# Performance work log

Hardware: AMD Instinct MI355X
Metric: run time of the kernel (lower is better)

The kernel has to match this reference:

```python
import jax, jax.numpy as jnp
import numpy as np

ITERS = 3  # iteration_num in the original module
B, L, H, N_LABELS = 16, 64, 512, 64


def setup_inputs() -> dict:
    key = jax.random.key(0)
    ks = jax.random.split(key, 11)
    s = H ** -0.5
    s2 = (2 * H) ** -0.5
    return {
        "h": jax.random.normal(ks[0], (B, L, H), jnp.float32),
        "c_slot": jax.random.normal(ks[1], (B, L, H), jnp.float32),
        "c_inte": jax.random.normal(ks[2], (B, H), jnp.float32),
        "W_SF": jax.random.normal(ks[3], (H, H), jnp.float32) * s,
        "V_SF": jax.random.normal(ks[4], (H, H), jnp.float32) * s,
        "V1_ID": jax.random.normal(ks[5], (H, H), jnp.float32) * s,
        "V2_ID_w": jax.random.normal(ks[6], (H, H), jnp.float32) * s,
        "V2_ID_b": jax.random.normal(ks[7], (H,), jnp.float32) * s,
        "W_ID": jax.random.normal(ks[8], (H, H), jnp.float32) * s,
        "W_inte_ans": jax.random.normal(ks[9], (N_LABELS, 2 * H), jnp.float32) * s2,
        "W_slot_ans": jax.random.normal(ks[10], (N_LABELS, 2 * H), jnp.float32) * s2,
    }


def reference(h, c_slot, c_inte, W_SF, V_SF, V1_ID, V2_ID_w, V2_ID_b, W_ID,
              W_inte_ans, W_slot_ans):
    # h, c_slot: [B,L,H]; c_inte: [B,H]
    # slot_features (V2_ID(h)) is loop-invariant in the original; hoisted.
    slot_features = h @ V2_ID_w.T + V2_ID_b  # [B,L,H]
    r_inte = c_inte
    r_slot = None
    for _ in range(ITERS):
        # f = sum_i V_SF(tanh(c_slot[:,i] + W_SF(r_inte))); V_SF linear -> sum first
        t = jnp.tanh(c_slot + (r_inte @ W_SF.T)[:, None, :])  # [B,L,H]
        f = t.sum(axis=1) @ V_SF.T  # [B,H]
        r_slot = f[:, None, :] * c_slot  # [B,L,H]
        hid = r_slot @ V1_ID.T  # [B,L,H]
        # pairwise additive attention scores, summed over batch AND hidden dims
        u = jnp.tanh(hid[:, :, None, :] + slot_features[:, None, :, :])  # [B,L,L,H]
        s = jnp.exp(jnp.einsum('bijh,gh->bijg', u, W_ID)).sum(axis=(0, 3))  # [L,L]
        atts = jnp.diagonal(s) / s.sum(axis=1)  # [L], scalar per position
        r = jnp.einsum('i,bih->bh', atts, r_slot)  # [B,H]
        r_inte = r + c_inte
    intent_output = jnp.concatenate([r_inte, h[:, -1, :]], axis=1) @ W_inte_ans.T  # [B,n_labels]
    slot_output = jnp.concatenate([h, r_slot], axis=-1) @ W_slot_ans.T  # [B,L,n_labels]
    return intent_output, slot_output
```

## Files before the change

### kernel.cpp

```cpp
#include <hip/hip_runtime.h>
#include <math.h>


typedef __attribute__((ext_vector_type(8))) short bf16x8;
typedef __attribute__((ext_vector_type(4))) float f32x4;

__device__ inline short f2bf(float x) {
  unsigned u = __float_as_uint(x);
  unsigned r = (u + 0x7fffu + ((u >> 16) & 1u)) >> 16;
  return (short)r;
}
__device__ inline float bf2f(short s) {
  return __uint_as_float(((unsigned)(unsigned short)s) << 16);
}
__device__ inline unsigned pack2(float a, float b) {
  return (__float_as_uint(a) >> 16) | (__float_as_uint(b) & 0xffff0000u);
}
__device__ inline float ftanh(float x) {
  float t = __expf(2.f * x);
  return 1.f - 2.f * __builtin_amdgcn_rcpf(t + 1.f);
}
__device__ inline void split8(float4 a, float4 b, bf16x8* hi, bf16x8* lo) {
  float xs[8] = {a.x, a.y, a.z, a.w, b.x, b.y, b.z, b.w};
  bf16x8 h, l;
#pragma unroll
  for (int e = 0; e < 8; ++e) {
    short hh = f2bf(xs[e]);
    h[e] = hh;
    l[e] = f2bf(xs[e] - bf2f(hh));
  }
  *hi = h;
  *lo = l;
}

__global__ __launch_bounds__(256) void k_lin1(
    const float* __restrict__ A, const float* __restrict__ rawB,
    const float* __restrict__ bias, float* __restrict__ C,
    const float* __restrict__ W_ID, const float* __restrict__ V1,
    const float* __restrict__ W_ia, const float* __restrict__ W_sa,
    const float* __restrict__ W_SF, const float* __restrict__ V_SF,
    short* __restrict__ wbp, short* __restrict__ v1h, short* __restrict__ v1l,
    float* __restrict__ wia_t, float* __restrict__ wsa_t,
    float* __restrict__ wsf_t, float* __restrict__ vsf_t,
    float* __restrict__ fzero) {
  __shared__ short Ah[2][512], Al[2][512];
  __shared__ float tile[64][65];
  const int nh = blockIdx.y;
  const int t = threadIdx.x;

  if (nh >= 4) {
    const int pid = (nh - 4) * 64 + blockIdx.x;
    if (pid < 256) {
#pragma unroll
      for (int e = 0; e < 4; ++e) {
        int idx = pid * 1024 + e * 256 + t;
        int j = idx & 7, lane = (idx >> 3) & 63;
        int ntile = (idx >> 9) & 31, kstep = idx >> 14;
        int g = ntile * 16 + (lane & 15);
        int h = kstep * 32 + (lane >> 4) * 8 + j;
        wbp[idx] = f2bf(W_ID[g * 512 + h]);
      }
    } else if (pid < 512) {
      int p = pid - 256;
#pragma unroll
      for (int e = 0; e < 4; ++e) {
        int idx = p * 1024 + e * 256 + t;
        int j = idx & 7, lane = (idx >> 3) & 63;
        int ntile = (idx >> 9) & 31, kstep = idx >> 14;
        int g = ntile * 16 + (lane & 15);
        int h = kstep * 32 + (lane >> 4) * 8 + j;
        float x = V1[g * 512 + h];
        short hi = f2bf(x);
        v1h[idx] = hi;
        v1l[idx] = f2bf(x - bf2f(hi));
      }
    } else if (pid < 672) {
      int p = pid - 512;
      const float* tin;
      float* tout;
      int R, C2, c0, r0;
      if (p < 64) {
        tin = W_SF; tout = wsf_t; R = 512; C2 = 512;
        c0 = (p & 7) * 64; r0 = (p >> 3) * 64;
      } else if (p < 128) {
        int q = p - 64;
        tin = V_SF; tout = vsf_t; R = 512; C2 = 512;
        c0 = (q & 7) * 64; r0 = (q >> 3) * 64;
      } else if (p < 144) {
        tin = W_ia; tout = wia_t; R = 64; C2 = 1024;
        c0 = (p - 128) * 64; r0 = 0;
      } else {
        tin = W_sa; tout = wsa_t; R = 64; C2 = 1024;
        c0 = (p - 144) * 64; r0 = 0;
      }
      const int tx = t & 63, ty = t >> 6;
#pragma unroll
      for (int it2 = 0; it2 < 16; ++it2) {
        int rl = ty + it2 * 4;
        tile[rl][tx] = tin[(r0 + rl) * C2 + c0 + tx];
      }
      __syncthreads();
#pragma unroll
      for (int it2 = 0; it2 < 16; ++it2) {
        int cl = ty + it2 * 4;
        tout[(c0 + cl) * R + r0 + tx] = tile[tx][cl];
      }
    }
    return;
  }

  const int m0 = blockIdx.x * 16;
  if (fzero && nh == 1 && blockIdx.x < 16) {
    fzero[blockIdx.x * 512 + t] = 0.f;
    fzero[blockIdx.x * 512 + 256 + t] = 0.f;
  }
  const int w = t >> 6, lane = t & 63;
  const int lq = lane >> 4, lm = lane & 15;
  f32x4 acc[2];
#pragma unroll
  for (int c = 0; c < 2; ++c) acc[c] = (f32x4){0.f, 0.f, 0.f, 0.f};

  const int nt0 = nh * 8 + w * 2;
  const float* vb0 = rawB + (nt0 * 16 + lm) * 512 + lq * 8;
  const float* vb1 = vb0 + 16 * 512;

  const int la = t >> 2, j0 = (t & 3) * 2;
  const int m = la & 15, kk = (la >> 4) * 8 + j0;
  const float* abase = A + (m0 + m) * 512 + kk;
  float2 x = *(const float2*)abase;

  for (int ks = 0; ks < 16; ++ks) {
    const int buf = ks & 1;
    float4 q0 = *(const float4*)(vb0 + ks * 32);
    float4 q1 = *(const float4*)(vb0 + ks * 32 + 4);
    float4 p0 = *(const float4*)(vb1 + ks * 32);
    float4 p1 = *(const float4*)(vb1 + ks * 32 + 4);
    float2 xn = x;
    if (ks < 15) xn = *(const float2*)(abase + (ks + 1) * 32);
    short h0 = f2bf(x.x), h1 = f2bf(x.y);
    short l0 = f2bf(x.x - bf2f(h0)), l1 = f2bf(x.y - bf2f(h1));
    *(short2*)&Ah[buf][t * 2] = make_short2(h0, h1);
    *(short2*)&Al[buf][t * 2] = make_short2(l0, l1);
    bf16x8 b0h, b0l, b1h, b1l;
    split8(q0, q1, &b0h, &b0l);
    split8(p0, p1, &b1h, &b1l);
    __syncthreads();
    bf16x8 ah = *(const bf16x8*)&Ah[buf][lane * 8];
    bf16x8 al = *(const bf16x8*)&Al[buf][lane * 8];
    acc[0] = __builtin_amdgcn_mfma_f32_16x16x32_bf16(ah, b0h, acc[0], 0, 0, 0);
    acc[0] = __builtin_amdgcn_mfma_f32_16x16x32_bf16(al, b0h, acc[0], 0, 0, 0);
    acc[0] = __builtin_amdgcn_mfma_f32_16x16x32_bf16(ah, b0l, acc[0], 0, 0, 0);
    acc[1] = __builtin_amdgcn_mfma_f32_16x16x32_bf16(ah, b1h, acc[1], 0, 0, 0);
    acc[1] = __builtin_amdgcn_mfma_f32_16x16x32_bf16(al, b1h, acc[1], 0, 0, 0);
    acc[1] = __builtin_amdgcn_mfma_f32_16x16x32_bf16(ah, b1l, acc[1], 0, 0, 0);
    x = xn;
  }
#pragma unroll
  for (int c = 0; c < 2; ++c)
#pragma unroll
    for (int reg = 0; reg < 4; ++reg) {
      int mm = m0 + lq * 4 + reg;
      int n = (nt0 + c) * 16 + lm;
      C[mm * 512 + n] = acc[c][reg] + bias[n];
    }
}

__global__ __launch_bounds__(256) void k_lin(const float* __restrict__ c_slot,
                                             const float* __restrict__ f,
                                             const short* __restrict__ bh,
                                             const short* __restrict__ bl,
                                             float* __restrict__ C,
                                             float* __restrict__ rs_out,
                                             float* __restrict__ smat0) {
  __shared__ short Ah[2][512], Al[2][512];
  __shared__ float fl[512];
  const int m0 = blockIdx.x * 16;
  const int nh = blockIdx.y;
  const int t = threadIdx.x;
  if (nh == 0 && blockIdx.x < 8) {
    smat0[blockIdx.x * 512 + t] = 0.f;
    smat0[blockIdx.x * 512 + 256 + t] = 0.f;
  }
  fl[t] = f[(blockIdx.x >> 2) * 512 + t];
  fl[t + 256] = f[(blockIdx.x >> 2) * 512 + 256 + t];
  const int w = t >> 6, lane = t & 63;
  const int lq = lane >> 4, lm = lane & 15;
  f32x4 acc[2];
#pragma unroll
  for (int c = 0; c < 2; ++c) acc[c] = (f32x4){0.f, 0.f, 0.f, 0.f};

  const bf16x8* gbh = (const bf16x8*)bh + (nh * 8 + w * 2) * 64 + lane;
  const bf16x8* gbl = (const bf16x8*)bl + (nh * 8 + w * 2) * 64 + lane;

  const int la = t >> 2, j0 = (t & 3) * 2;
  const int m = la & 15, kk = (la >> 4) * 8 + j0;
  const float* abase = c_slot + (m0 + m) * 512 + kk;
  float* rbase = rs_out + (m0 + m) * 512 + kk;
  __syncthreads();
  float2 x = *(const float2*)abase;

  for (int ks = 0; ks < 16; ++ks) {
    const int buf = ks & 1;
    bf16x8 b0h = gbh[ks * 2048];
    bf16x8 b1h = gbh[ks * 2048 + 64];
    bf16x8 b0l = gbl[ks * 2048];
    bf16x8 b1l = gbl[ks * 2048 + 64];
    float2 xn = x;
    if (ks < 15) xn = *(const float2*)(abase + (ks + 1) * 32);
    float a0 = x.x * fl[ks * 32 + kk];
    float a1 = x.y * fl[ks * 32 + kk + 1];
    if (nh == 0) *(float2*)(rbase + ks * 32) = make_float2(a0, a1);
    short h0 = f2bf(a0), h1 = f2bf(a1);
    short l0 = f2bf(a0 - bf2f(h0)), l1 = f2bf(a1 - bf2f(h1));
    *(short2*)&Ah[buf][t * 2] = make_short2(h0, h1);
    *(short2*)&Al[buf][t * 2] = make_short2(l0, l1);
    __syncthreads();
    bf16x8 ah = *(const bf16x8*)&Ah[buf][lane * 8];
    bf16x8 al = *(const bf16x8*)&Al[buf][lane * 8];
    acc[0] = __builtin_amdgcn_mfma_f32_16x16x32_bf16(ah, b0h, acc[0], 0, 0, 0);
    acc[0] = __builtin_amdgcn_mfma_f32_16x16x32_bf16(al, b0h, acc[0], 0, 0, 0);
    acc[0] = __builtin_amdgcn_mfma_f32_16x16x32_bf16(ah, b0l, acc[0], 0, 0, 0);
    acc[1] = __builtin_amdgcn_mfma_f32_16x16x32_bf16(ah, b1h, acc[1], 0, 0, 0);
    acc[1] = __builtin_amdgcn_mfma_f32_16x16x32_bf16(al, b1h, acc[1], 0, 0, 0);
    acc[1] = __builtin_amdgcn_mfma_f32_16x16x32_bf16(ah, b1l, acc[1], 0, 0, 0);
    x = xn;
  }
#pragma unroll
  for (int c = 0; c < 2; ++c)
#pragma unroll
    for (int reg = 0; reg < 4; ++reg) {
      int mm = m0 + lq * 4 + reg;
      int n = nh * 128 + (w * 2 + c) * 16 + lm;
      C[mm * 512 + n] = acc[c][reg];
    }
}

__global__ __launch_bounds__(512) void k_mid(int first,
                                             const float* __restrict__ smat,
                                             const float* __restrict__ r_slot,
                                             const float* __restrict__ c_inte,
                                             const float* __restrict__ c_slot,
                                             const float* __restrict__ wsf_t,
                                             const float* __restrict__ vsf_t,
                                             float* __restrict__ f) {
  __shared__ float av[64];
  __shared__ float riv[512];
  __shared__ float red[512];
  __shared__ float tm[64], ts[64];
  const int b = blockIdx.x >> 3, hc = blockIdx.x & 7;
  const int t = threadIdx.x;
  const int hl = t & 63, kq = t >> 6;

  if (first) {
    riv[t] = c_inte[b * 512 + t];
  } else {
    if (t < 256) {
      int w = t >> 6, lane = t & 63;
      for (int r = w * 16; r < w * 16 + 16; ++r) {
        float v = smat[r * 64 + lane];
        float s = v;
        s += __shfl_xor(s, 1);
        s += __shfl_xor(s, 2);
        s += __shfl_xor(s, 4);
        s += __shfl_xor(s, 8);
        s += __shfl_xor(s, 16);
        s += __shfl_xor(s, 32);
        float d = __shfl(v, r);
        if (lane == 0) av[r] = d / s;
      }
    }
    __syncthreads();
    float a = 0.f;
    const float* rp = r_slot + b * 64 * 512 + t;
#pragma unroll 8
    for (int i = 0; i < 64; ++i) a += av[i] * rp[i * 512];
    riv[t] = a + c_inte[b * 512 + t];
  }
  __syncthreads();
  {
    const float* wp = wsf_t + hc * 64 + hl;
    float p = 0.f;
#pragma unroll 8
    for (int k = kq * 64; k < kq * 64 + 64; ++k) p += riv[k] * wp[k * 512];
    red[t] = p;
  }
  __syncthreads();
  if (t < 64) {
    float s = 0.f;
#pragma unroll
    for (int q = 0; q < 8; ++q) s += red[q * 64 + t];
    tm[t] = s;
  }
  __syncthreads();
  {
    float tmph = tm[hl];
    const float* cp = c_slot + (b * 64 + kq * 8) * 512 + hc * 64 + hl;
    float s = 0.f;
#pragma unroll
    for (int l = 0; l < 8; ++l) s += ftanh(cp[l * 512] + tmph);
    red[t] = s;
  }
  __syncthreads();
  if (t < 64) {
    float s = 0.f;
#pragma unroll
    for (int q = 0; q < 8; ++q) s += red[q * 64 + t];
    ts[t] = s;
  }
  __syncthreads();
  {
    const float* vp = vsf_t + (hc * 64) * 512 + t;
    float p = 0.f;
#pragma unroll 8
    for (int k = 0; k < 64; ++k) p += ts[k] * vp[k * 512];
    atomicAdd(&f[b * 512 + t], p);
  }
}

__global__ __launch_bounds__(512, 4) void k_score(const float* __restrict__ hid,
                                                  const float* __restrict__ sf,
                                                  const short* __restrict__ wbp,
                                                  float* __restrict__ smat,
                                                  float* __restrict__ fz,
                                                  float* __restrict__ oz) {
  __shared__ short As[16][2048];
  __shared__ float red[8][64];
  const int i = blockIdx.x, b = blockIdx.y;
  const int t = threadIdx.x;
  if (fz && i == 0) fz[b * 512 + t] = 0.f;
  if (oz && i == 1 && b < 2) oz[b * 512 + t] = 0.f;
  const int w = t >> 6, lane = t & 63;
  const int lq = lane >> 4, lm = lane & 15;

  f32x4 acc[4][4];
#pragma unroll
  for (int r = 0; r < 4; ++r)
#pragma unroll
    for (int c = 0; c < 4; ++c) acc[r][c] = (f32x4){0.f, 0.f, 0.f, 0.f};

  const float* hrow = hid + (b * 64 + i) * 512;
  const float* sfb = sf + b * 64 * 512;

  const int fid = t >> 1, half = t & 1;
  const int am = (fid >> 6) * 16 + (fid & 15);
  const int ak = ((fid >> 4) & 3) * 8 + half * 4;
  const int aoff = fid * 8 + half * 4;

  const float* hp0 = hrow + ak;
  const float* sp0 = sfb + am * 512 + ak;

  const bf16x8* gb = (const bf16x8*)wbp + (w * 4) * 64 + lane;
  bf16x8 nb0 = gb[0];
  bf16x8 nb1 = gb[64];
  bf16x8 nb2 = gb[128];
  bf16x8 nb3 = gb[192];

#pragma unroll 4
  for (int ks = 0; ks < 16; ++ks) {
    float4 hv = *(const float4*)(hp0 + ks * 32);
    float4 sv = *(const float4*)(sp0 + ks * 32);
    uint2 pk;
    pk.x = pack2(ftanh(hv.x + sv.x), ftanh(hv.y + sv.y));
    pk.y = pack2(ftanh(hv.z + sv.z), ftanh(hv.w + sv.w));
    *(uint2*)&As[ks][aoff] = pk;
  }
  __syncthreads();

  for (int ks = 0; ks < 16; ++ks) {
    bf16x8 b0 = nb0, b1 = nb1, b2 = nb2, b3 = nb3;
    if (ks < 15) {
      nb0 = gb[(ks + 1) * 2048];
      nb1 = gb[(ks + 1) * 2048 + 64];
      nb2 = gb[(ks + 1) * 2048 + 128];
      nb3 = gb[(ks + 1) * 2048 + 192];
    }
    bf16x8 af0 = *(const bf16x8*)&As[ks][(0 * 64 + lane) * 8];
    bf16x8 af1 = *(const bf16x8*)&As[ks][(1 * 64 + lane) * 8];
    bf16x8 af2 = *(const bf16x8*)&As[ks][(2 * 64 + lane) * 8];
    bf16x8 af3 = *(const bf16x8*)&As[ks][(3 * 64 + lane) * 8];
    acc[0][0] = __builtin_amdgcn_mfma_f32_16x16x32_bf16(af0, b0, acc[0][0], 0, 0, 0);
    acc[1][0] = __builtin_amdgcn_mfma_f32_16x16x32_bf16(af1, b0, acc[1][0], 0, 0, 0);
    acc[2][0] = __builtin_amdgcn_mfma_f32_16x16x32_bf16(af2, b0, acc[2][0], 0, 0, 0);
    acc[3][0] = __builtin_amdgcn_mfma_f32_16x16x32_bf16(af3, b0, acc[3][0], 0, 0, 0);
    acc[0][1] = __builtin_amdgcn_mfma_f32_16x16x32_bf16(af0, b1, acc[0][1], 0, 0, 0);
    acc[1][1] = __builtin_amdgcn_mfma_f32_16x16x32_bf16(af1, b1, acc[1][1], 0, 0, 0);
    acc[2][1] = __builtin_amdgcn_mfma_f32_16x16x32_bf16(af2, b1, acc[2][1], 0, 0, 0);
    acc[3][1] = __builtin_amdgcn_mfma_f32_16x16x32_bf16(af3, b1, acc[3][1], 0, 0, 0);
    acc[0][2] = __builtin_amdgcn_mfma_f32_16x16x32_bf16(af0, b2, acc[0][2], 0, 0, 0);
    acc[1][2] = __builtin_amdgcn_mfma_f32_16x16x32_bf16(af1, b2, acc[1][2], 0, 0, 0);
    acc[2][2] = __builtin_amdgcn_mfma_f32_16x16x32_bf16(af2, b2, acc[2][2], 0, 0, 0);
    acc[3][2] = __builtin_amdgcn_mfma_f32_16x16x32_bf16(af3, b2, acc[3][2], 0, 0, 0);
    acc[0][3] = __builtin_amdgcn_mfma_f32_16x16x32_bf16(af0, b3, acc[0][3], 0, 0, 0);
    acc[1][3] = __builtin_amdgcn_mfma_f32_16x16x32_bf16(af1, b3, acc[1][3], 0, 0, 0);
    acc[2][3] = __builtin_amdgcn_mfma_f32_16x16x32_bf16(af2, b3, acc[2][3], 0, 0, 0);
    acc[3][3] = __builtin_amdgcn_mfma_f32_16x16x32_bf16(af3, b3, acc[3][3], 0, 0, 0);
  }

#pragma unroll
  for (int r = 0; r < 4; ++r) {
#pragma unroll
    for (int reg = 0; reg < 4; ++reg) {
      float v = __expf(acc[r][0][reg]) + __expf(acc[r][1][reg]) +
                __expf(acc[r][2][reg]) + __expf(acc[r][3][reg]);
      v += __shfl_down(v, 8, 16);
      v += __shfl_down(v, 4, 16);
      v += __shfl_down(v, 2, 16);
      v += __shfl_down(v, 1, 16);
      if (lm == 0) red[w][r * 16 + lq * 4 + reg] = v;
    }
  }
  __syncthreads();
  if (t < 64) {
    float s = 0.f;
#pragma unroll
    for (int ww = 0; ww < 8; ++ww) s += red[ww][t];
    atomicAdd(&smat[i * 64 + t], s);
  }
}

__global__ __launch_bounds__(256) void k_post(const float* __restrict__ smat,
                                              const float* __restrict__ r_slot,
                                              const float* __restrict__ c_inte,
                                              const float* __restrict__ h,
                                              const float* __restrict__ wia_t,
                                              const float* __restrict__ wsa_t,
                                              float* __restrict__ out) {
  __shared__ float av[64], riv[64], red[256];
  const int t = threadIdx.x;
  if (blockIdx.x < 256) {
    int idx = blockIdx.x * 256 + t;
    int ml = idx >> 6, n = idx & 63;
    const float* x1 = h + ml * 512;
    const float* x2 = r_slot + ml * 512;
    float acc = 0.f;
    for (int k = 0; k < 512; k += 4) {
      float4 x = *(const float4*)(x1 + k);
      acc += x.x * wsa_t[k * 64 + n] + x.y * wsa_t[(k + 1) * 64 + n] +
             x.z * wsa_t[(k + 2) * 64 + n] + x.w * wsa_t[(k + 3) * 64 + n];
    }
    for (int k = 0; k < 512; k += 4) {
      float4 x = *(const float4*)(x2 + k);
      acc += x.x * wsa_t[(512 + k) * 64 + n] + x.y * wsa_t[(513 + k) * 64 + n] +
             x.z * wsa_t[(514 + k) * 64 + n] + x.w * wsa_t[(515 + k) * 64 + n];
    }
    out[1024 + idx] = acc;
  } else {
    const int bb = blockIdx.x - 256;
    const int b = bb >> 3, kc = bb & 7;
    const int w = t >> 6, lane = t & 63;
    for (int r = w * 16; r < w * 16 + 16; ++r) {
      float v = smat[r * 64 + lane];
      float s = v;
      s += __shfl_xor(s, 1);
      s += __shfl_xor(s, 2);
      s += __shfl_xor(s, 4);
      s += __shfl_xor(s, 8);
      s += __shfl_xor(s, 16);
      s += __shfl_xor(s, 32);
      float d = __shfl(v, r);
      if (lane == 0) av[r] = d / s;
    }
    __syncthreads();
    {
      const int hh = kc * 64 + lane;
      float a = 0.f;
      const float* rp = r_slot + (b * 64 + w * 16) * 512 + hh;
#pragma unroll
      for (int i = 0; i < 16; ++i) a += av[w * 16 + i] * rp[i * 512];
      red[t] = a;
    }
    __syncthreads();
    if (t < 64)
      riv[t] = red[t] + red[t + 64] + red[t + 128] + red[t + 192] +
               c_inte[b * 512 + kc * 64 + t];
    __syncthreads();
    {
      const int n = lane;
      const float* hrow = h + (b * 64 + 63) * 512 + kc * 64;
      float p = 0.f;
#pragma unroll
      for (int k = w * 16; k < w * 16 + 16; ++k) {
        p += riv[k] * wia_t[(kc * 64 + k) * 64 + n];
        p += hrow[k] * wia_t[(512 + kc * 64 + k) * 64 + n];
      }
      red[t] = p;
    }
    __syncthreads();
    if (t < 64)
      atomicAdd(&out[b * 64 + t],
                red[t] + red[t + 64] + red[t + 128] + red[t + 192]);
  }
}

extern "C" void kernel_launch(void* const* d_in, const int* in_sizes, int n_in,
                              void* d_out, int out_size, void* d_ws, size_t ws_size,
                              hipStream_t stream) {
  const float* h      = (const float*)d_in[0];
  const float* c_slot = (const float*)d_in[1];
  const float* c_inte = (const float*)d_in[2];
  const float* W_SF   = (const float*)d_in[3];
  const float* V_SF   = (const float*)d_in[4];
  const float* V1_ID  = (const float*)d_in[5];
  const float* V2_w   = (const float*)d_in[6];
  const float* V2_b   = (const float*)d_in[7];
  const float* W_ID   = (const float*)d_in[8];
  const float* W_ia   = (const float*)d_in[9];
  const float* W_sa   = (const float*)d_in[10];
  float* out = (float*)d_out;

  float* ws     = (float*)d_ws;
  short* wbp    = (short*)ws;
  short* v1h    = (short*)(ws + 393216);
  short* v1l    = (short*)(ws + 524288);
  float* sfbuf  = ws + 655360;
  float* r_slot = ws + 1179648;
  float* hid    = ws + 1703936;
  float* smat   = ws + 2228224;
  float* f      = ws + 2232320;
  float* wia_t  = ws + 2240512;
  float* wsa_t  = ws + 2306048;
  float* wsf_t  = ws + 2371584;
  float* vsf_t  = ws + 2633728;

  k_lin1<<<dim3(64, 15), 256, 0, stream>>>(h, V2_w, V2_b, sfbuf,
                                           W_ID, V1_ID, W_ia, W_sa, W_SF, V_SF,
                                           wbp, v1h, v1l,
                                           wia_t, wsa_t, wsf_t, vsf_t, f);

  for (int it = 0; it < 3; ++it) {
    k_mid<<<128, 512, 0, stream>>>(it == 0 ? 1 : 0, smat, r_slot, c_inte,
                                   c_slot, wsf_t, vsf_t, f);
    k_lin<<<dim3(64, 4), 256, 0, stream>>>(c_slot, f, v1h, v1l,
                                           hid, r_slot, smat);
    k_score<<<dim3(64, 16), 512, 0, stream>>>(hid, sfbuf, wbp, smat, f,
                                              it == 2 ? out : nullptr);
  }

  k_post<<<384, 256, 0, stream>>>(smat, r_slot, c_inte, h, wia_t, wsa_t, out);
}
```

Before: 300.1 us.

## Fold first-iteration f computation into setup kernel and slot output into score

The first iteration's f (tanh-sum over c_slot plus the V_SF projection) is now computed inside the setup kernel as per-chunk partials, which k_lin sums, so the first k_mid launch is skipped. The slot-output GEMV moves from k_post into extra blocks of the last k_score launch, so it runs alongside the score work and k_post shrinks to the intent-output part. The aim is fewer launches and less serial tail work, at the cost of untransposed, less coalesced weight reads in the setup blocks.

```diff
diff --git a/kernel.cpp b/kernel.cpp
--- a/kernel.cpp
+++ b/kernel.cpp
@@ -39,12 +39,14 @@
     const float* __restrict__ W_ID, const float* __restrict__ V1,
     const float* __restrict__ W_ia, const float* __restrict__ W_sa,
     const float* __restrict__ W_SF, const float* __restrict__ V_SF,
+    const float* __restrict__ c_inte, const float* __restrict__ c_slot,
     short* __restrict__ wbp, short* __restrict__ v1h, short* __restrict__ v1l,
     float* __restrict__ wia_t, float* __restrict__ wsa_t,
     float* __restrict__ wsf_t, float* __restrict__ vsf_t,
-    float* __restrict__ fzero) {
+    float* __restrict__ fp) {
   __shared__ short Ah[2][512], Al[2][512];
   __shared__ float tile[64][65];
+  __shared__ float riv2[512], red2[256], tm2[64], ts2[64];
   const int nh = blockIdx.y;
   const int t = threadIdx.x;
 
@@ -105,15 +107,58 @@
         int cl = ty + it2 * 4;
         tout[(c0 + cl) * R + r0 + tx] = tile[tx][cl];
       }
+    } else if (pid < 800) {
+      const int q = pid - 672;
+      const int b = q >> 3, hc = q & 7;
+      const int hl = t & 63, kq = t >> 6;
+      riv2[t] = c_inte[b * 512 + t];
+      riv2[t + 256] = c_inte[b * 512 + 256 + t];
+      __syncthreads();
+      {
+        const float* wrow = W_SF + (hc * 64 + hl) * 512 + kq * 128;
+        float p = 0.f;
+#pragma unroll 8
+        for (int k = 0; k < 128; k += 4) {
+          float4 wv = *(const float4*)(wrow + k);
+          p += wv.x * riv2[kq * 128 + k] + wv.y * riv2[kq * 128 + k + 1] +
+               wv.z * riv2[kq * 128 + k + 2] + wv.w * riv2[kq * 128 + k + 3];
+        }
+        red2[t] = p;
+      }
+      __syncthreads();
+      if (t < 64) tm2[t] = red2[t] + red2[t + 64] + red2[t + 128] + red2[t + 192];
+      __syncthreads();
+      {
+        float tmph = tm2[hl];
+        const float* cp = c_slot + (b * 64 + kq * 16) * 512 + hc * 64 + hl;
+        float s = 0.f;
+#pragma unroll
+        for (int l = 0; l < 16; ++l) s += ftanh(cp[l * 512] + tmph);
+        red2[t] = s;
+      }
+      __syncthreads();
+      if (t < 64) ts2[t] = red2[t] + red2[t + 64] + red2[t + 128] + red2[t + 192];
+      __syncthreads();
+      {
+#pragma unroll
+        for (int half = 0; half < 2; ++half) {
+          int to = t + half * 256;
+          const float* vrow = V_SF + to * 512 + hc * 64;
+          float p = 0.f;
+#pragma unroll 8
+          for (int k = 0; k < 64; k += 4) {
+            float4 vv = *(const float4*)(vrow + k);
+            p += vv.x * ts2[k] + vv.y * ts2[k + 1] + vv.z * ts2[k + 2] +
+                 vv.w * ts2[k + 3];
+          }
+          fp[(b * 8 + hc) * 512 + to] = p;
+        }
+      }
     }
     return;
   }
 
   const int m0 = blockIdx.x * 16;
-  if (fzero && nh == 1 && blockIdx.x < 16) {
-    fzero[blockIdx.x * 512 + t] = 0.f;
-    fzero[blockIdx.x * 512 + 256 + t] = 0.f;
-  }
   const int w = t >> 6, lane = t & 63;
   const int lq = lane >> 4, lm = lane & 15;
   f32x4 acc[2];
@@ -167,6 +212,8 @@
 
 __global__ __launch_bounds__(256) void k_lin(const float* __restrict__ c_slot,
                                              const float* __restrict__ f,
+                                             const float* __restrict__ fp,
+                                             int use_fp,
                                              const short* __restrict__ bh,
                                              const short* __restrict__ bl,
                                              float* __restrict__ C,
@@ -181,8 +228,20 @@
     smat0[blockIdx.x * 512 + t] = 0.f;
     smat0[blockIdx.x * 512 + 256 + t] = 0.f;
   }
-  fl[t] = f[(blockIdx.x >> 2) * 512 + t];
-  fl[t + 256] = f[(blockIdx.x >> 2) * 512 + 256 + t];
+  if (use_fp) {
+    const float* fb = fp + (blockIdx.x >> 2) * 8 * 512;
+    float s0 = 0.f, s1 = 0.f;
+#pragma unroll
+    for (int hc = 0; hc < 8; ++hc) {
+      s0 += fb[hc * 512 + t];
+      s1 += fb[hc * 512 + 256 + t];
+    }
+    fl[t] = s0;
+    fl[t + 256] = s1;
+  } else {
+    fl[t] = f[(blockIdx.x >> 2) * 512 + t];
+    fl[t + 256] = f[(blockIdx.x >> 2) * 512 + 256 + t];
+  }
   const int w = t >> 6, lane = t & 63;
   const int lq = lane >> 4, lm = lane & 15;
   f32x4 acc[2];
@@ -317,16 +376,37 @@
   }
 }
 
-__global__ __launch_bounds__(512, 4) void k_score(const float* __restrict__ hid,
-                                                  const float* __restrict__ sf,
-                                                  const short* __restrict__ wbp,
-                                                  float* __restrict__ smat,
-                                                  float* __restrict__ fz,
-                                                  float* __restrict__ oz) {
+__global__ __launch_bounds__(512, 4) void k_score(
+    const float* __restrict__ hid, const float* __restrict__ sf,
+    const short* __restrict__ wbp, float* __restrict__ smat,
+    float* __restrict__ fz, float* __restrict__ oz,
+    const float* __restrict__ hin, const float* __restrict__ r_slot,
+    const float* __restrict__ wsa_t) {
   __shared__ short As[16][2048];
   __shared__ float red[8][64];
   const int i = blockIdx.x, b = blockIdx.y;
   const int t = threadIdx.x;
+
+  if (b >= 16) {
+    int idx = ((b - 16) * 64 + i) * 512 + t;
+    int ml = idx >> 6, n = idx & 63;
+    const float* x1 = hin + ml * 512;
+    const float* x2 = r_slot + ml * 512;
+    float acc = 0.f;
+    for (int k = 0; k < 512; k += 4) {
+      float4 x = *(const float4*)(x1 + k);
+      acc += x.x * wsa_t[k * 64 + n] + x.y * wsa_t[(k + 1) * 64 + n] +
+             x.z * wsa_t[(k + 2) * 64 + n] + x.w * wsa_t[(k + 3) * 64 + n];
+    }
+    for (int k = 0; k < 512; k += 4) {
+      float4 x = *(const float4*)(x2 + k);
+      acc += x.x * wsa_t[(512 + k) * 64 + n] + x.y * wsa_t[(513 + k) * 64 + n] +
+             x.z * wsa_t[(514 + k) * 64 + n] + x.w * wsa_t[(515 + k) * 64 + n];
+    }
+    oz[1024 + idx] = acc;
+    return;
+  }
+
   if (fz && i == 0) fz[b * 512 + t] = 0.f;
   if (oz && i == 1 && b < 2) oz[b * 512 + t] = 0.f;
   const int w = t >> 6, lane = t & 63;
@@ -423,73 +503,53 @@
                                               const float* __restrict__ c_inte,
                                               const float* __restrict__ h,
                                               const float* __restrict__ wia_t,
-                                              const float* __restrict__ wsa_t,
                                               float* __restrict__ out) {
   __shared__ float av[64], riv[64], red[256];
   const int t = threadIdx.x;
-  if (blockIdx.x < 256) {
-    int idx = blockIdx.x * 256 + t;
-    int ml = idx >> 6, n = idx & 63;
-    const float* x1 = h + ml * 512;
-    const float* x2 = r_slot + ml * 512;
-    float acc = 0.f;
-    for (int k = 0; k < 512; k += 4) {
-      float4 x = *(const float4*)(x1 + k);
-      acc += x.x * wsa_t[k * 64 + n] + x.y * wsa_t[(k + 1) * 64 + n] +
-             x.z * wsa_t[(k + 2) * 64 + n] + x.w * wsa_t[(k + 3) * 64 + n];
-    }
-    for (int k = 0; k < 512; k += 4) {
-      float4 x = *(const float4*)(x2 + k);
-      acc += x.x * wsa_t[(512 + k) * 64 + n] + x.y * wsa_t[(513 + k) * 64 + n] +
-             x.z * wsa_t[(514 + k) * 64 + n] + x.w * wsa_t[(515 + k) * 64 + n];
-    }
-    out[1024 + idx] = acc;
-  } else {
-    const int bb = blockIdx.x - 256;
-    const int b = bb >> 3, kc = bb & 7;
-    const int w = t >> 6, lane = t & 63;
-    for (int r = w * 16; r < w * 16 + 16; ++r) {
-      float v = smat[r * 64 + lane];
-      float s = v;
-      s += __shfl_xor(s, 1);
-      s += __shfl_xor(s, 2);
-      s += __shfl_xor(s, 4);
-      s += __shfl_xor(s, 8);
-      s += __shfl_xor(s, 16);
-      s += __shfl_xor(s, 32);
-      float d = __shfl(v, r);
-      if (lane == 0) av[r] = d / s;
-    }
-    __syncthreads();
-    {
-      const int hh = kc * 64 + lane;
-      float a = 0.f;
-      const float* rp = r_slot + (b * 64 + w * 16) * 512 + hh;
-#pragma unroll
-      for (int i = 0; i < 16; ++i) a += av[w * 16 + i] * rp[i * 512];
-      red[t] = a;
-    }
-    __syncthreads();
-    if (t < 64)
-      riv[t] = red[t] + red[t + 64] + red[t + 128] + red[t + 192] +
-               c_inte[b * 512 + kc * 64 + t];
-    __syncthreads();
-    {
-      const int n = lane;
-      const float* hrow = h + (b * 64 + 63) * 512 + kc * 64;
-      float p = 0.f;
-#pragma unroll
-      for (int k = w * 16; k < w * 16 + 16; ++k) {
-        p += riv[k] * wia_t[(kc * 64 + k) * 64 + n];
-        p += hrow[k] * wia_t[(512 + kc * 64 + k) * 64 + n];
-      }
-      red[t] = p;
-    }
-    __syncthreads();
-    if (t < 64)
-      atomicAdd(&out[b * 64 + t],
-                red[t] + red[t + 64] + red[t + 128] + red[t + 192]);
-  }
+  const int bb = blockIdx.x;
+  const int b = bb >> 3, kc = bb & 7;
+  const int w = t >> 6, lane = t & 63;
+  for (int r = w * 16; r < w * 16 + 16; ++r) {
+    float v = smat[r * 64 + lane];
+    float s = v;
+    s += __shfl_xor(s, 1);
+    s += __shfl_xor(s, 2);
+    s += __shfl_xor(s, 4);
+    s += __shfl_xor(s, 8);
+    s += __shfl_xor(s, 16);
+    s += __shfl_xor(s, 32);
+    float d = __shfl(v, r);
+    if (lane == 0) av[r] = d / s;
+  }
+  __syncthreads();
+  {
+    const int hh = kc * 64 + lane;
+    float a = 0.f;
+    const float* rp = r_slot + (b * 64 + w * 16) * 512 + hh;
+#pragma unroll
+    for (int i = 0; i < 16; ++i) a += av[w * 16 + i] * rp[i * 512];
+    red[t] = a;
+  }
+  __syncthreads();
+  if (t < 64)
+    riv[t] = red[t] + red[t + 64] + red[t + 128] + red[t + 192] +
+             c_inte[b * 512 + kc * 64 + t];
+  __syncthreads();
+  {
+    const int n = lane;
+    const float* hrow = h + (b * 64 + 63) * 512 + kc * 64;
+    float p = 0.f;
+#pragma unroll
+    for (int k = w * 16; k < w * 16 + 16; ++k) {
+      p += riv[k] * wia_t[(kc * 64 + k) * 64 + n];
+      p += hrow[k] * wia_t[(512 + kc * 64 + k) * 64 + n];
+    }
+    red[t] = p;
+  }
+  __syncthreads();
+  if (t < 64)
+    atomicAdd(&out[b * 64 + t],
+              red[t] + red[t + 64] + red[t + 128] + red[t + 192]);
 }
 
 extern "C" void kernel_launch(void* const* d_in, const int* in_sizes, int n_in,
@@ -510,6 +570,7 @@
 
   float* ws     = (float*)d_ws;
   short* wbp    = (short*)ws;
+  float* fpart  = ws + 131072;
   short* v1h    = (short*)(ws + 393216);
   short* v1l    = (short*)(ws + 524288);
   float* sfbuf  = ws + 655360;
@@ -522,19 +583,22 @@
   float* wsf_t  = ws + 2371584;
   float* vsf_t  = ws + 2633728;
 
-  k_lin1<<<dim3(64, 15), 256, 0, stream>>>(h, V2_w, V2_b, sfbuf,
+  k_lin1<<<dim3(64, 17), 256, 0, stream>>>(h, V2_w, V2_b, sfbuf,
                                            W_ID, V1_ID, W_ia, W_sa, W_SF, V_SF,
+                                           c_inte, c_slot,
                                            wbp, v1h, v1l,
-                                           wia_t, wsa_t, wsf_t, vsf_t, f);
+                                           wia_t, wsa_t, wsf_t, vsf_t, fpart);
 
   for (int it = 0; it < 3; ++it) {
-    k_mid<<<128, 512, 0, stream>>>(it == 0 ? 1 : 0, smat, r_slot, c_inte,
-                                   c_slot, wsf_t, vsf_t, f);
-    k_lin<<<dim3(64, 4), 256, 0, stream>>>(c_slot, f, v1h, v1l,
-                                           hid, r_slot, smat);
-    k_score<<<dim3(64, 16), 512, 0, stream>>>(hid, sfbuf, wbp, smat, f,
-                                              it == 2 ? out : nullptr);
-  }
-
-  k_post<<<384, 256, 0, stream>>>(smat, r_slot, c_inte, h, wia_t, wsa_t, out);
-}
+    if (it > 0)
+      k_mid<<<128, 512, 0, stream>>>(0, smat, r_slot, c_inte, c_slot,
+                                     wsf_t, vsf_t, f);
+    k_lin<<<dim3(64, 4), 256, 0, stream>>>(c_slot, f, fpart, it == 0 ? 1 : 0,
+                                           v1h, v1l, hid, r_slot, smat);
+    k_score<<<dim3(64, it == 2 ? 18 : 16), 512, 0, stream>>>(
+        hid, sfbuf, wbp, smat, f, it == 2 ? out : nullptr,
+        h, r_slot, wsa_t);
+  }
+
+  k_post<<<128, 256, 0, stream>>>(smat, r_slot, c_inte, h, wia_t, out);
+}
```

Measured after the change: 314.1 us. 1.05x slower.
